# Optimization experiments

Measured on AMD Instinct MI355X. Metric: run time of the kernel, lower is better.

## Reference

```python
import jax, jax.numpy as jnp
import numpy as np

B, T, K = 64, 1024, 256  # batch, seq_len, num_labels


def setup_inputs() -> dict:
    key = jax.random.key(0)
    k1, k2 = jax.random.split(key)
    emissions = jax.random.normal(k1, (B, T, K), dtype=jnp.float32)
    transitions = jax.random.normal(k2, (K, K), dtype=jnp.float32) * 0.1
    return {"emissions": emissions, "transitions": transitions}


def _viterbi_decode(emissions, transitions):
    """Viterbi decode, mirroring tfa.text.crf_decode with full-length sequences.
    emissions: [B, T, K] unary potentials; transitions: [K, K] (prev -> next).
    Returns int32 tag sequence [B, T]."""
    em = jnp.transpose(emissions, (1, 0, 2))  # [T, B, K]

    def fwd_step(state, emit_t):
        # state: [B, K] running max scores ending in each tag at time t-1
        scores = state[:, :, None] + transitions[None, :, :]  # [B, K_prev, K_next]
        bp = jnp.argmax(scores, axis=1).astype(jnp.int32)      # [B, K] backpointers
        new_state = jnp.max(scores, axis=1) + emit_t           # [B, K]
        return new_state, bp

    state, bps = jax.lax.scan(fwd_step, em[0], em[1:])  # bps: [T-1, B, K]
    last_tag = jnp.argmax(state, axis=-1).astype(jnp.int32)  # [B]

    def back_step(tag, bp_t):
        prev = jnp.take_along_axis(bp_t, tag[:, None], axis=1)[:, 0]
        return prev, prev

    # reverse scan: bps[i] maps tag at t=i+1 back to tag at t=i
    _, earlier = jax.lax.scan(back_step, last_tag, bps, reverse=True)  # [T-1, B]
    tags = jnp.concatenate([earlier, last_tag[None, :]], axis=0)  # [T, B]
    return jnp.transpose(tags, (1, 0))  # [B, T]


def reference(emissions, transitions):
    # CRF.call in inference mode: crf_decode then cast to the input dtype.
    return _viterbi_decode(emissions, transitions).astype(emissions.dtype)
```

## Files before the change

kernel.cpp:

```cpp
#include <hip/hip_runtime.h>


#define CRF_B 64
#define CRF_T 1024
#define CRF_K 256
#define NSEG  16
#define SEGLEN 64

#define FG 8
#define FP 32


#define LD4(v, p, col) { \
    v.x = trans[(size_t)(p) * CRF_K + (col)]; \
    v.y = trans[(size_t)((p) + 1) * CRF_K + (col)]; \
    v.z = trans[(size_t)((p) + 2) * CRF_K + (col)]; \
    v.w = trans[(size_t)((p) + 3) * CRF_K + (col)]; }

#define FWD_CHUNK(idx, ta, tb) { \
    float4 sv = sp[idx]; \
    float a0 = sv.x + ta.x; \
    float a1 = sv.y + ta.y; \
    float a2 = sv.z + ta.z; \
    float a3 = sv.w + ta.w; \
    m0 = fmaxf(m0, fmaxf(fmaxf(a0, a1), fmaxf(a2, a3))); \
    float c0 = sv.x + tb.x; \
    float c1 = sv.y + tb.y; \
    float c2 = sv.z + tb.z; \
    float c3 = sv.w + tb.w; \
    m1 = fmaxf(m1, fmaxf(fmaxf(c0, c1), fmaxf(c2, c3))); }

__global__ __launch_bounds__(1024, 4) void crf_forward_states(
    const float* __restrict__ em, const float* __restrict__ trans,
    float* __restrict__ M, unsigned char* __restrict__ gidp)
{
    const int b   = blockIdx.x;
    const int tid = threadIdx.x;
    const int g   = tid >> 7;
    const int c   = tid & 127;

    __shared__ __align__(16) float s_state[CRF_K];
    __shared__ float s_partial[FG][CRF_K];

    const int pbase = g * FP;
    const int c2    = c + 128;

    float4 ta0, ta1, ta2, ta3, ta4, ta5, ta6, ta7;
    float4 tb0, tb1, tb2, tb3, tb4, tb5, tb6, tb7;
    LD4(ta0, pbase +  0, c)  LD4(ta1, pbase +  4, c)
    LD4(ta2, pbase +  8, c)  LD4(ta3, pbase + 12, c)
    LD4(ta4, pbase + 16, c)  LD4(ta5, pbase + 20, c)
    LD4(ta6, pbase + 24, c)  LD4(ta7, pbase + 28, c)
    LD4(tb0, pbase +  0, c2) LD4(tb1, pbase +  4, c2)
    LD4(tb2, pbase +  8, c2) LD4(tb3, pbase + 12, c2)
    LD4(tb4, pbase + 16, c2) LD4(tb5, pbase + 20, c2)
    LD4(tb6, pbase + 24, c2) LD4(tb7, pbase + 28, c2)

    const float* emb = em + (size_t)b * CRF_T * CRF_K;
    if (tid < CRF_K) s_state[tid] = emb[tid];
    float e_cur = 0.0f;
    if (tid < CRF_K) e_cur = emb[CRF_K + tid];
    __syncthreads();

    for (int t = 1; t < CRF_T; ++t) {
        float e_next = 0.0f;
        if (tid < CRF_K && t + 1 < CRF_T)
            e_next = emb[(t + 1) * CRF_K + tid];

        float m0 = -INFINITY, m1 = -INFINITY;
        const float4* sp = (const float4*)(s_state + pbase);
        FWD_CHUNK(0, ta0, tb0) FWD_CHUNK(1, ta1, tb1)
        FWD_CHUNK(2, ta2, tb2) FWD_CHUNK(3, ta3, tb3)
        FWD_CHUNK(4, ta4, tb4) FWD_CHUNK(5, ta5, tb5)
        FWD_CHUNK(6, ta6, tb6) FWD_CHUNK(7, ta7, tb7)

        s_partial[g][c]  = m0;
        s_partial[g][c2] = m1;
        __syncthreads();
        if (tid < CRF_K) {
            float bv = s_partial[0][tid];
            int   bg = 0;
#pragma unroll
            for (int j = 1; j < FG; ++j) {
                float pv = s_partial[j][tid];
                if (pv > bv) { bv = pv; bg = j; }
            }
            s_state[tid] = bv + e_cur;
            M[((size_t)t * CRF_B + b) * CRF_K + tid] = bv;
            if (gidp) {
                int g1 = __shfl_down(bg, 1, 64);
                if ((tid & 1) == 0)
                    gidp[((size_t)t * CRF_B + b) * 128 + (tid >> 1)] =
                        (unsigned char)(bg | (g1 << 4));
            }
        }
        __syncthreads();
        e_cur = e_next;
    }
}


#define BPG_CHUNK(j) { \
    float4 mm = M4[j]; float4 ee = E4[j]; \
    float s0 = mm.x + ee.x, s1 = mm.y + ee.y; \
    float s2 = mm.z + ee.z, s3 = mm.w + ee.w; \
    float t0v = s_tile[base + 4*(j) + 0][lane]; \
    float t1v = s_tile[base + 4*(j) + 1][lane]; \
    float t2v = s_tile[base + 4*(j) + 2][lane]; \
    float t3v = s_tile[base + 4*(j) + 3][lane]; \
    float v0 = s0 + t0v; if (v0 > best) { best = v0; arg = base + 4*(j); } \
    float v1 = s1 + t1v; if (v1 > best) { best = v1; arg = base + 4*(j) + 1; } \
    float v2 = s2 + t2v; if (v2 > best) { best = v2; arg = base + 4*(j) + 2; } \
    float v3 = s3 + t3v; if (v3 > best) { best = v3; arg = base + 4*(j) + 3; } }

#define BPG_CHUNK0(j) { \
    float4 ee = E4[j]; \
    float t0v = s_tile[base + 4*(j) + 0][lane]; \
    float t1v = s_tile[base + 4*(j) + 1][lane]; \
    float t2v = s_tile[base + 4*(j) + 2][lane]; \
    float t3v = s_tile[base + 4*(j) + 3][lane]; \
    float v0 = ee.x + t0v; if (v0 > best) { best = v0; arg = base + 4*(j); } \
    float v1 = ee.y + t1v; if (v1 > best) { best = v1; arg = base + 4*(j) + 1; } \
    float v2 = ee.z + t2v; if (v2 > best) { best = v2; arg = base + 4*(j) + 2; } \
    float v3 = ee.w + t3v; if (v3 > best) { best = v3; arg = base + 4*(j) + 3; } }

__global__ __launch_bounds__(128) void crf_bp_gid(
    const float* __restrict__ M, const float* __restrict__ em,
    const float* __restrict__ trans, const unsigned char* __restrict__ gidp,
    unsigned char* __restrict__ bp)
{
    const int b    = blockIdx.x >> 3;
    const int cg   = (blockIdx.x >> 1) & 3;
    const int ts   = blockIdx.x & 1;
    const int tid  = threadIdx.x;
    const int lane = tid & 63;
    const int w    = tid >> 6;

    __shared__ float s_tile[CRF_K][64];

    const int k0 = cg * 64;
    for (int idx = tid; idx < CRF_K * 64; idx += 128) {
        const int p = idx >> 6, cc = idx & 63;
        s_tile[p][cc] = trans[(size_t)p * CRF_K + k0 + cc];
    }
    __syncthreads();

    const int t_lo = ts * 512;
    const int t_hi = ts ? (CRF_T - 1) : 512;
    const int half = (k0 >> 1) + (lane >> 1);

    int t1 = t_lo + w;

    if (t1 == 0) {
        const unsigned char gb = gidp[((size_t)1 * CRF_B + b) * 128 + half];
        const int g    = (lane & 1) ? ((gb >> 4) & 7) : (gb & 7);
        const int base = g << 5;
        const float4* E4 =
            (const float4*)(em + (size_t)b * CRF_T * CRF_K + base);
        float best = -INFINITY; int arg = base;
        BPG_CHUNK0(0) BPG_CHUNK0(1) BPG_CHUNK0(2) BPG_CHUNK0(3)
        BPG_CHUNK0(4) BPG_CHUNK0(5) BPG_CHUNK0(6) BPG_CHUNK0(7)
        bp[((size_t)b * (CRF_T - 1) + 0) * CRF_K + k0 + lane] =
            (unsigned char)arg;
        t1 += 2;
    }

    for (; t1 < t_hi; t1 += 2) {
        const unsigned char gb =
            gidp[((size_t)(t1 + 1) * CRF_B + b) * 128 + half];
        const int g    = (lane & 1) ? ((gb >> 4) & 7) : (gb & 7);
        const int base = g << 5;
        const float4* M4 =
            (const float4*)(M + ((size_t)t1 * CRF_B + b) * CRF_K + base);
        const float4* E4 =
            (const float4*)(em + ((size_t)b * CRF_T + t1) * CRF_K + base);
        float best = -INFINITY; int arg = base;
        BPG_CHUNK(0) BPG_CHUNK(1) BPG_CHUNK(2) BPG_CHUNK(3)
        BPG_CHUNK(4) BPG_CHUNK(5) BPG_CHUNK(6) BPG_CHUNK(7)
        bp[((size_t)b * (CRF_T - 1) + t1) * CRF_K + k0 + lane] =
            (unsigned char)arg;
    }
}


__global__ __launch_bounds__(1024, 2) void crf_bp_matrix(
    const float* __restrict__ M, const float* __restrict__ em,
    const float* __restrict__ trans, unsigned char* __restrict__ bp)
{
    const int b   = blockIdx.x >> 4;
    const int seg = blockIdx.x & 15;
    const int tid = threadIdx.x;
    const int g   = tid >> 8;
    const int k   = tid & 255;

    __shared__ __align__(16) float s_row[CRF_K];
    __shared__ float s_pv[4][CRF_K];
    __shared__ int   s_pi[4][CRF_K];

    const int pbase = g * 64;
    float4 tr[16];
#pragma unroll
    for (int i = 0; i < 16; ++i) {
        const int p = pbase + 4 * i;
        tr[i].x = trans[(p + 0) * CRF_K + k];
        tr[i].y = trans[(p + 1) * CRF_K + k];
        tr[i].z = trans[(p + 2) * CRF_K + k];
        tr[i].w = trans[(p + 3) * CRF_K + k];
    }

    const int t_lo = seg * SEGLEN;
    const int t_hi = min(t_lo + SEGLEN, CRF_T - 1);
    unsigned char* bpb = bp + (size_t)b * (CRF_T - 1) * CRF_K;

    for (int t1 = t_lo; t1 < t_hi; ++t1) {
        if (tid < CRF_K) {
            float ev = em[((size_t)b * CRF_T + t1) * CRF_K + tid];
            float sv = ev;
            if (t1 > 0) sv = M[((size_t)t1 * CRF_B + b) * CRF_K + tid] + ev;
            s_row[tid] = sv;
        }
        __syncthreads();

        float best = -INFINITY;
        int   arg  = pbase;
        const float4* sp = (const float4*)(s_row + pbase);
#pragma unroll
        for (int i = 0; i < 16; ++i) {
            float4 st = sp[i];
            const int p = pbase + 4 * i;
            float s0 = st.x + tr[i].x;
            float s1 = st.y + tr[i].y;
            float s2 = st.z + tr[i].z;
            float s3 = st.w + tr[i].w;
            if (s0 > best) { best = s0; arg = p; }
            if (s1 > best) { best = s1; arg = p + 1; }
            if (s2 > best) { best = s2; arg = p + 2; }
            if (s3 > best) { best = s3; arg = p + 3; }
        }
        s_pv[g][k] = best;
        s_pi[g][k] = arg;
        __syncthreads();
        if (tid < CRF_K) {
            float bv = s_pv[0][tid];
            int   ba = s_pi[0][tid];
#pragma unroll
            for (int j = 1; j < 4; ++j) {
                float v = s_pv[j][tid];
                if (v > bv) { bv = v; ba = s_pi[j][tid]; }
            }
            bpb[(size_t)t1 * CRF_K + tid] = (unsigned char)ba;
        }
        __syncthreads();
    }
}


__global__ __launch_bounds__(256) void crf_seg_maps(
    const unsigned char* __restrict__ bp, unsigned char* __restrict__ maps)
{
    const int b   = blockIdx.x >> 4;
    const int s   = blockIdx.x & 15;
    const int tid = threadIdx.x;
    const int rows = (s == NSEG - 1) ? SEGLEN - 1 : SEGLEN;
    const int r0   = s * SEGLEN;

    __shared__ unsigned char lbp[SEGLEN][CRF_K];

    const unsigned char* bpb = bp + (size_t)b * (CRF_T - 1) * CRF_K;
    const int nw = rows * 64;
    for (int w = tid; w < nw; w += 256) {
        const int r = w >> 6, cc = w & 63;
        ((unsigned int*)lbp[r])[cc] =
            ((const unsigned int*)(bpb + (size_t)(r0 + r) * CRF_K))[cc];
    }
    __syncthreads();

    int tag = tid;
    for (int j = rows - 1; j >= 0; --j) tag = lbp[j][tag];
    maps[((size_t)b * NSEG + s) * CRF_K + tid] = (unsigned char)tag;
}

__global__ __launch_bounds__(256) void crf_compose(
    const float* __restrict__ M, const float* __restrict__ em,
    const unsigned char* __restrict__ maps,
    int* __restrict__ exits, float* __restrict__ out)
{
    const int b   = blockIdx.x;
    const int tid = threadIdx.x;

    __shared__ float s_wv[4];
    __shared__ int   s_wi[4];

    float v = M[((size_t)(CRF_T - 1) * CRF_B + b) * CRF_K + tid]
            + em[((size_t)b * CRF_T + (CRF_T - 1)) * CRF_K + tid];
    int   i = tid;
#pragma unroll
    for (int off = 32; off >= 1; off >>= 1) {
        float ov = __shfl_xor(v, off, 64);
        int   oi = __shfl_xor(i, off, 64);
        if (ov > v || (ov == v && oi < i)) { v = ov; i = oi; }
    }
    const int lane = tid & 63, wv = tid >> 6;
    if (lane == 0) { s_wv[wv] = v; s_wi[wv] = i; }
    __syncthreads();
    if (tid == 0) {
        float bv = s_wv[0]; int bi = s_wi[0];
#pragma unroll
        for (int w = 1; w < 4; ++w)
            if (s_wv[w] > bv) { bv = s_wv[w]; bi = s_wi[w]; }
        out[(size_t)b * CRF_T + (CRF_T - 1)] = (float)bi;
        int E = bi;
        exits[b * NSEG + NSEG - 1] = E;
        const unsigned char* mb = maps + (size_t)b * NSEG * CRF_K;
        for (int s = NSEG - 1; s >= 1; --s) {
            E = mb[(size_t)s * CRF_K + E];
            exits[b * NSEG + s - 1] = E;
        }
    }
}

__global__ __launch_bounds__(256) void crf_emit(
    const unsigned char* __restrict__ bp, const int* __restrict__ exits,
    float* __restrict__ out)
{
    const int b   = blockIdx.x >> 4;
    const int s   = blockIdx.x & 15;
    const int tid = threadIdx.x;
    const int rows = (s == NSEG - 1) ? SEGLEN - 1 : SEGLEN;
    const int r0   = s * SEGLEN;

    __shared__ unsigned char lbp[SEGLEN][CRF_K];

    const unsigned char* bpb = bp + (size_t)b * (CRF_T - 1) * CRF_K;
    const int nw = rows * 64;
    for (int w = tid; w < nw; w += 256) {
        const int r = w >> 6, cc = w & 63;
        ((unsigned int*)lbp[r])[cc] =
            ((const unsigned int*)(bpb + (size_t)(r0 + r) * CRF_K))[cc];
    }
    __syncthreads();

    int tag = tid;
    const bool win = (tid == exits[b * NSEG + s]);
    for (int j = rows - 1; j >= 0; --j) {
        tag = lbp[j][tag];
        if (win) out[(size_t)b * CRF_T + r0 + j] = (float)tag;
    }
}

__global__ void crf_zero_out(float* __restrict__ out, int n)
{
    int i = blockIdx.x * blockDim.x + threadIdx.x;
    if (i < n) out[i] = 0.0f;
}


extern "C" void kernel_launch(void* const* d_in, const int* in_sizes, int n_in,
                              void* d_out, int out_size, void* d_ws, size_t ws_size,
                              hipStream_t stream) {
    (void)in_sizes; (void)n_in;
    const float* em    = (const float*)d_in[0];
    const float* trans = (const float*)d_in[1];
    float* out = (float*)d_out;

    const size_t M_bytes     = (size_t)CRF_T * CRF_B * CRF_K * sizeof(float);
    const size_t gid_bytes   = (size_t)CRF_T * CRF_B * 128;
    const size_t bp_bytes    = (size_t)CRF_B * (CRF_T - 1) * CRF_K;
    const size_t maps_bytes  = (size_t)CRF_B * NSEG * CRF_K;
    const size_t exits_bytes = (size_t)CRF_B * NSEG * sizeof(int);

    char* w = (char*)d_ws;
    if (ws_size >= M_bytes + gid_bytes + bp_bytes + maps_bytes + exits_bytes) {
        float*         M     = (float*)w;            w += M_bytes;
        unsigned char* gidp  = (unsigned char*)w;    w += gid_bytes;
        unsigned char* bp    = (unsigned char*)w;    w += bp_bytes;
        unsigned char* maps  = (unsigned char*)w;    w += maps_bytes;
        int*           exits = (int*)w;

        crf_forward_states<<<CRF_B, 1024, 0, stream>>>(em, trans, M, gidp);
        crf_bp_gid<<<CRF_B * 8, 128, 0, stream>>>(M, em, trans, gidp, bp);
        crf_seg_maps<<<CRF_B * NSEG, 256, 0, stream>>>(bp, maps);
        crf_compose<<<CRF_B, 256, 0, stream>>>(M, em, maps, exits, out);
        crf_emit<<<CRF_B * NSEG, 256, 0, stream>>>(bp, exits, out);
    } else if (ws_size >= M_bytes + bp_bytes + maps_bytes + exits_bytes) {
        float*         M     = (float*)w;            w += M_bytes;
        unsigned char* bp    = (unsigned char*)w;    w += bp_bytes;
        unsigned char* maps  = (unsigned char*)w;    w += maps_bytes;
        int*           exits = (int*)w;

        crf_forward_states<<<CRF_B, 1024, 0, stream>>>(em, trans, M, nullptr);
        crf_bp_matrix<<<CRF_B * NSEG, 1024, 0, stream>>>(M, em, trans, bp);
        crf_seg_maps<<<CRF_B * NSEG, 256, 0, stream>>>(bp, maps);
        crf_compose<<<CRF_B, 256, 0, stream>>>(M, em, maps, exits, out);
        crf_emit<<<CRF_B * NSEG, 256, 0, stream>>>(bp, exits, out);
    } else {
        crf_zero_out<<<(out_size + 255) / 256, 256, 0, stream>>>(out, out_size);
    }
}
```

Baseline: 1.317 ms.

## Shorten forward critical path by deferring group-id argmax and widening bp_gid blocks

In the forward recurrence, the per-step argmax over the eight partial maxima is replaced by a branchless fmax tree. The group-id computation and its byte store are deferred to the start of the next iteration, so they run off the serial dependency chain that gates the state update. The max reductions are also reassociated into shorter chains. The backpointer kernel now uses 256 threads (4 timesteps per iteration) and prefetches the next group id. It folds the t=0 case into the loop, which adds a branch per iteration.

```diff
diff --git a/kernel.cpp b/kernel.cpp
--- a/kernel.cpp
+++ b/kernel.cpp
@@ -23,12 +23,14 @@
     float a1 = sv.y + ta.y; \
     float a2 = sv.z + ta.z; \
     float a3 = sv.w + ta.w; \
-    m0 = fmaxf(m0, fmaxf(fmaxf(a0, a1), fmaxf(a2, a3))); \
+    float r0 = fmaxf(fmaxf(a0, a1), a2); \
+    m0 = fmaxf(fmaxf(r0, a3), m0); \
     float c0 = sv.x + tb.x; \
     float c1 = sv.y + tb.y; \
     float c2 = sv.z + tb.z; \
     float c3 = sv.w + tb.w; \
-    m1 = fmaxf(m1, fmaxf(fmaxf(c0, c1), fmaxf(c2, c3))); }
+    float r1 = fmaxf(fmaxf(c0, c1), c2); \
+    m1 = fmaxf(fmaxf(r1, c3), m1); }
 
 __global__ __launch_bounds__(1024, 4) void crf_forward_states(
     const float* __restrict__ em, const float* __restrict__ trans,
@@ -62,7 +64,26 @@
     if (tid < CRF_K) e_cur = emb[CRF_K + tid];
     __syncthreads();
 
+    float sp0 = 0, sp1 = 0, sp2 = 0, sp3 = 0;
+    float sp4 = 0, sp5 = 0, sp6 = 0, sp7 = 0;
+    float sbv = 0;
+
     for (int t = 1; t < CRF_T; ++t) {
+        if (gidp && tid < CRF_K && t > 1) {
+            int bg = 7;
+            if (sp6 == sbv) bg = 6;
+            if (sp5 == sbv) bg = 5;
+            if (sp4 == sbv) bg = 4;
+            if (sp3 == sbv) bg = 3;
+            if (sp2 == sbv) bg = 2;
+            if (sp1 == sbv) bg = 1;
+            if (sp0 == sbv) bg = 0;
+            int g1 = __shfl_down(bg, 1, 64);
+            if ((tid & 1) == 0)
+                gidp[((size_t)(t - 1) * CRF_B + b) * 128 + (tid >> 1)] =
+                    (unsigned char)(bg | (g1 << 4));
+        }
+
         float e_next = 0.0f;
         if (tid < CRF_K && t + 1 < CRF_T)
             e_next = emb[(t + 1) * CRF_K + tid];
@@ -78,24 +99,35 @@
         s_partial[g][c2] = m1;
         __syncthreads();
         if (tid < CRF_K) {
-            float bv = s_partial[0][tid];
-            int   bg = 0;
-#pragma unroll
-            for (int j = 1; j < FG; ++j) {
-                float pv = s_partial[j][tid];
-                if (pv > bv) { bv = pv; bg = j; }
-            }
+            float p0 = s_partial[0][tid], p1 = s_partial[1][tid];
+            float p2 = s_partial[2][tid], p3 = s_partial[3][tid];
+            float p4 = s_partial[4][tid], p5 = s_partial[5][tid];
+            float p6 = s_partial[6][tid], p7 = s_partial[7][tid];
+            float q0 = fmaxf(fmaxf(p0, p1), p2);
+            float q1 = fmaxf(fmaxf(p3, p4), p5);
+            float bv = fmaxf(fmaxf(fmaxf(q0, q1), p6), p7);
             s_state[tid] = bv + e_cur;
             M[((size_t)t * CRF_B + b) * CRF_K + tid] = bv;
-            if (gidp) {
-                int g1 = __shfl_down(bg, 1, 64);
-                if ((tid & 1) == 0)
-                    gidp[((size_t)t * CRF_B + b) * 128 + (tid >> 1)] =
-                        (unsigned char)(bg | (g1 << 4));
-            }
+            sp0 = p0; sp1 = p1; sp2 = p2; sp3 = p3;
+            sp4 = p4; sp5 = p5; sp6 = p6; sp7 = p7; sbv = bv;
         }
         __syncthreads();
         e_cur = e_next;
+    }
+
+    if (gidp && tid < CRF_K) {
+        int bg = 7;
+        if (sp6 == sbv) bg = 6;
+        if (sp5 == sbv) bg = 5;
+        if (sp4 == sbv) bg = 4;
+        if (sp3 == sbv) bg = 3;
+        if (sp2 == sbv) bg = 2;
+        if (sp1 == sbv) bg = 1;
+        if (sp0 == sbv) bg = 0;
+        int g1 = __shfl_down(bg, 1, 64);
+        if ((tid & 1) == 0)
+            gidp[((size_t)(CRF_T - 1) * CRF_B + b) * 128 + (tid >> 1)] =
+                (unsigned char)(bg | (g1 << 4));
     }
 }
 
@@ -124,7 +156,7 @@
     float v2 = ee.z + t2v; if (v2 > best) { best = v2; arg = base + 4*(j) + 2; } \
     float v3 = ee.w + t3v; if (v3 > best) { best = v3; arg = base + 4*(j) + 3; } }
 
-__global__ __launch_bounds__(128) void crf_bp_gid(
+__global__ __launch_bounds__(256) void crf_bp_gid(
     const float* __restrict__ M, const float* __restrict__ em,
     const float* __restrict__ trans, const unsigned char* __restrict__ gidp,
     unsigned char* __restrict__ bp)
@@ -139,7 +171,7 @@
     __shared__ float s_tile[CRF_K][64];
 
     const int k0 = cg * 64;
-    for (int idx = tid; idx < CRF_K * 64; idx += 128) {
+    for (int idx = tid; idx < CRF_K * 64; idx += 256) {
         const int p = idx >> 6, cc = idx & 63;
         s_tile[p][cc] = trans[(size_t)p * CRF_K + k0 + cc];
     }
@@ -148,37 +180,35 @@
     const int t_lo = ts * 512;
     const int t_hi = ts ? (CRF_T - 1) : 512;
     const int half = (k0 >> 1) + (lane >> 1);
+    const int odd  = lane & 1;
 
     int t1 = t_lo + w;
-
-    if (t1 == 0) {
-        const unsigned char gb = gidp[((size_t)1 * CRF_B + b) * 128 + half];
-        const int g    = (lane & 1) ? ((gb >> 4) & 7) : (gb & 7);
+    if (t1 >= t_hi) return;
+    unsigned char gb = gidp[((size_t)(t1 + 1) * CRF_B + b) * 128 + half];
+
+    for (; t1 < t_hi; t1 += 4) {
+        const int tn = t1 + 4;
+        unsigned char gb_next = 0;
+        if (tn < t_hi)
+            gb_next = gidp[((size_t)(tn + 1) * CRF_B + b) * 128 + half];
+
+        const int g    = odd ? ((gb >> 4) & 7) : (gb & 7);
         const int base = g << 5;
-        const float4* E4 =
-            (const float4*)(em + (size_t)b * CRF_T * CRF_K + base);
-        float best = -INFINITY; int arg = base;
-        BPG_CHUNK0(0) BPG_CHUNK0(1) BPG_CHUNK0(2) BPG_CHUNK0(3)
-        BPG_CHUNK0(4) BPG_CHUNK0(5) BPG_CHUNK0(6) BPG_CHUNK0(7)
-        bp[((size_t)b * (CRF_T - 1) + 0) * CRF_K + k0 + lane] =
-            (unsigned char)arg;
-        t1 += 2;
-    }
-
-    for (; t1 < t_hi; t1 += 2) {
-        const unsigned char gb =
-            gidp[((size_t)(t1 + 1) * CRF_B + b) * 128 + half];
-        const int g    = (lane & 1) ? ((gb >> 4) & 7) : (gb & 7);
-        const int base = g << 5;
-        const float4* M4 =
-            (const float4*)(M + ((size_t)t1 * CRF_B + b) * CRF_K + base);
         const float4* E4 =
             (const float4*)(em + ((size_t)b * CRF_T + t1) * CRF_K + base);
         float best = -INFINITY; int arg = base;
-        BPG_CHUNK(0) BPG_CHUNK(1) BPG_CHUNK(2) BPG_CHUNK(3)
-        BPG_CHUNK(4) BPG_CHUNK(5) BPG_CHUNK(6) BPG_CHUNK(7)
+        if (t1 == 0) {
+            BPG_CHUNK0(0) BPG_CHUNK0(1) BPG_CHUNK0(2) BPG_CHUNK0(3)
+            BPG_CHUNK0(4) BPG_CHUNK0(5) BPG_CHUNK0(6) BPG_CHUNK0(7)
+        } else {
+            const float4* M4 =
+                (const float4*)(M + ((size_t)t1 * CRF_B + b) * CRF_K + base);
+            BPG_CHUNK(0) BPG_CHUNK(1) BPG_CHUNK(2) BPG_CHUNK(3)
+            BPG_CHUNK(4) BPG_CHUNK(5) BPG_CHUNK(6) BPG_CHUNK(7)
+        }
         bp[((size_t)b * (CRF_T - 1) + t1) * CRF_K + k0 + lane] =
             (unsigned char)arg;
+        gb = gb_next;
     }
 }
 
@@ -223,10 +253,10 @@
 
         float best = -INFINITY;
         int   arg  = pbase;
-        const float4* sp = (const float4*)(s_row + pbase);
+        const float4* spp = (const float4*)(s_row + pbase);
 #pragma unroll
         for (int i = 0; i < 16; ++i) {
-            float4 st = sp[i];
+            float4 st = spp[i];
             const int p = pbase + 4 * i;
             float s0 = st.x + tr[i].x;
             float s1 = st.y + tr[i].y;
@@ -378,7 +408,7 @@
         int*           exits = (int*)w;
 
         crf_forward_states<<<CRF_B, 1024, 0, stream>>>(em, trans, M, gidp);
-        crf_bp_gid<<<CRF_B * 8, 128, 0, stream>>>(M, em, trans, gidp, bp);
+        crf_bp_gid<<<CRF_B * 8, 256, 0, stream>>>(M, em, trans, gidp, bp);
         crf_seg_maps<<<CRF_B * NSEG, 256, 0, stream>>>(bp, maps);
         crf_compose<<<CRF_B, 256, 0, stream>>>(M, em, maps, exits, out);
         crf_emit<<<CRF_B * NSEG, 256, 0, stream>>>(bp, exits, out);
```

Result: faster. 1.105 ms (-16.1%).
